# Performance work log

Hardware: AMD Instinct MI355X
Metric: run time of the kernel (lower is better)

The kernel has to match this reference:

```python
import jax, jax.numpy as jnp
import numpy as np

B, L, C = 32, 64, 4


def setup_inputs() -> dict:
    key = jax.random.key(0)
    k_idx, k0, k1, k2, k3 = jax.random.split(key, 5)
    # One-hot encoded sequences, flattened to (B, L*C) as the layer expects.
    idx = jax.random.randint(k_idx, (B, L), 0, C)
    x_lc = jax.nn.one_hot(idx, C, dtype=jnp.float32).reshape(B, L * C)
    return {
        "x_lc": x_lc,
        "theta_0": jnp.zeros((1,), dtype=jnp.float32),  # Constant(0.0) init
        "theta_1": 0.05 * jax.random.normal(k1, (L, C), dtype=jnp.float32),
        "theta_2": 0.05 * jax.random.normal(k2, (L, C, L, C), dtype=jnp.float32),
        "theta_3": 0.05 * jax.random.normal(k3, (L, C, L, C, L, C), dtype=jnp.float32),
    }


def reference(x_lc, theta_0, theta_1, theta_2, theta_3):
    Lp, Cp = theta_1.shape
    xr = x_lc.reshape(-1, Lp, Cp)  # (B, L, C)
    pos = jnp.arange(Lp)
    # strict upper-triangular position masks: l0 < l1 (< l2)
    m2 = (pos[None, :] > pos[:, None]).astype(theta_2.dtype)      # (L, L)
    m3 = m2[:, :, None] * m2[None, :, :]                           # (L, L, L)
    # order 1: sum_{l,c} theta_1[l,c] x[b,l,c]
    phi = theta_0[0] + jnp.einsum('ua,bua->b', theta_1, xr)
    # order 2: sum over l0<l1 of theta_2 * x x
    phi = phi + jnp.einsum('uavc,uv,bua,bvc->b', theta_2, m2, xr, xr)
    # order 3: sum over l0<l1<l2 of theta_3 * x x x
    phi = phi + jnp.einsum('uavcwe,uvw,bua,bvc,bwe->b', theta_3, m3, xr, xr, xr)
    return phi.reshape(-1, 1)
```

## Files before the change

kernel.cpp:

```cpp
#include <hip/hip_runtime.h>

#define BB 32
#define LL 64
#define LC 256
#define NPAIR 2016
#define WSTRIDE 2048

__global__ __launch_bounds__(256) void pair_kernel(
    const float* __restrict__ x, const float* __restrict__ t2,
    const float* __restrict__ t3, float* __restrict__ ws2)
{
    const int t = blockIdx.x;
    int v = (int)((1.0f + sqrtf(8.0f * (float)t + 1.0f)) * 0.5f);
    while (v * (v - 1) / 2 > t) --v;
    while ((v + 1) * v / 2 <= t) ++v;
    const int u = t - v * (v - 1) / 2;

    const int tid = threadIdx.x;
    const int b = tid >> 3, k = tid & 7;
    const float4* __restrict__ x4 = (const float4*)x + b * 64;

    int c[8];
#pragma unroll
    for (int m = 0; m < 8; ++m) {
        float4 f = x4[8 * m + k];
        int ci = 0; float best = f.x;
        if (f.y > best) { best = f.y; ci = 1; }
        if (f.z > best) { best = f.z; ci = 2; }
        if (f.w > best) { best = f.w; ci = 3; }
        c[m] = ci;
    }
    float4 fu = x4[u], fv = x4[v];
    int cu = 0; { float bst = fu.x;
        if (fu.y > bst) { bst = fu.y; cu = 1; }
        if (fu.z > bst) { bst = fu.z; cu = 2; }
        if (fu.w > bst) { bst = fu.w; cu = 3; } }
    int cv = 0; { float bst = fv.x;
        if (fv.y > bst) { bst = fv.y; cv = 1; }
        if (fv.z > bst) { bst = fv.z; cv = 2; }
        if (fv.w > bst) { bst = fv.w; cv = 3; } }
    const int pu = 4 * u + cu, pv = 4 * v + cv;

    const float4* __restrict__ row4 =
        (const float4*)(t3 + ((size_t)pu << 16) + ((size_t)pv << 8));

    float acc = 0.0f;
    const int mstart = (v + 1 - k + 7) >> 3;
#pragma unroll
    for (int m = 0; m < 8; ++m) {
        if (m >= mstart) {
            float4 f = row4[8 * m + k];
            float s0 = (c[m] & 2) ? f.z : f.x;
            float s1 = (c[m] & 2) ? f.w : f.y;
            acc += (c[m] & 1) ? s1 : s0;
        }
    }
    acc += __shfl_down(acc, 4, 8);
    acc += __shfl_down(acc, 2, 8);
    acc += __shfl_down(acc, 1, 8);
    if (k == 0) ws2[b * WSTRIDE + t] = acc + t2[pu * LC + pv];
}

__global__ __launch_bounds__(256) void reduce_kernel(
    const float* __restrict__ x, const float* __restrict__ t0,
    const float* __restrict__ t1, const float* __restrict__ ws2,
    float* __restrict__ out)
{
    const int b = blockIdx.x;
    const int tid = threadIdx.x;
    const float* __restrict__ wsb = ws2 + b * WSTRIDE;
    float v = 0.0f;
    for (int t = tid; t < NPAIR; t += 256) v += wsb[t];
    if (tid < LL) {
        float4 f = ((const float4*)x)[b * 64 + tid];
        int c = 0; float best = f.x;
        if (f.y > best) { best = f.y; c = 1; }
        if (f.z > best) { best = f.z; c = 2; }
        if (f.w > best) { best = f.w; c = 3; }
        v += t1[4 * tid + c];
    }
    for (int off = 32; off > 0; off >>= 1) v += __shfl_down(v, off, 64);
    __shared__ float wsum[4];
    if ((tid & 63) == 0) wsum[tid >> 6] = v;
    __syncthreads();
    if (tid == 0) out[b] = wsum[0] + wsum[1] + wsum[2] + wsum[3] + t0[0];
}

extern "C" void kernel_launch(void* const* d_in, const int* in_sizes, int n_in,
                              void* d_out, int out_size, void* d_ws, size_t ws_size,
                              hipStream_t stream) {
    const float* x  = (const float*)d_in[0];
    const float* t0 = (const float*)d_in[1];
    const float* t1 = (const float*)d_in[2];
    const float* t2 = (const float*)d_in[3];
    const float* t3 = (const float*)d_in[4];
    float* out = (float*)d_out;
    float* ws2 = (float*)d_ws;

    pair_kernel<<<NPAIR, 256, 0, stream>>>(x, t2, t3, ws2);
    reduce_kernel<<<BB, 256, 0, stream>>>(x, t0, t1, ws2, out);
}
```

Measured before the change: 104.7 us.

## Fuse pair and reduce kernels with atomics, process four pairs per block

Merges the two-kernel pipeline into one kernel that walks four consecutive (u,v) pairs per block, reuses the decoded one-hot codes across them, and accumulates straight into the output with atomicAdd after a memset. The aim is to remove the workspace round trip and the second launch, and to cut per-block setup relative to the useful gathers. In exchange there are 504 blocks instead of 2016, which lowers parallelism for the memory-bound gathers, adds a memset launch, and introduces contended atomics on 32 outputs.

Result: slower. 115.5 us (+10.3%).

```diff
diff --git a/kernel.cpp b/kernel.cpp
--- a/kernel.cpp
+++ b/kernel.cpp
@@ -4,18 +4,15 @@
 #define LL 64
 #define LC 256
 #define NPAIR 2016
-#define WSTRIDE 2048
+#define PPB 4
+#define NBLK (NPAIR / PPB)
 
-__global__ __launch_bounds__(256) void pair_kernel(
-    const float* __restrict__ x, const float* __restrict__ t2,
-    const float* __restrict__ t3, float* __restrict__ ws2)
+__global__ __launch_bounds__(256) void fused_kernel(
+    const float* __restrict__ x, const float* __restrict__ t0,
+    const float* __restrict__ t1, const float* __restrict__ t2,
+    const float* __restrict__ t3, float* __restrict__ out)
 {
-    const int t = blockIdx.x;
-    int v = (int)((1.0f + sqrtf(8.0f * (float)t + 1.0f)) * 0.5f);
-    while (v * (v - 1) / 2 > t) --v;
-    while ((v + 1) * v / 2 <= t) ++v;
-    const int u = t - v * (v - 1) / 2;
-
+    const int g = blockIdx.x;
     const int tid = threadIdx.x;
     const int b = tid >> 3, k = tid & 7;
     const float4* __restrict__ x4 = (const float4*)x + b * 64;
@@ -30,60 +27,57 @@
         if (f.w > best) { best = f.w; ci = 3; }
         c[m] = ci;
     }
-    float4 fu = x4[u], fv = x4[v];
-    int cu = 0; { float bst = fu.x;
-        if (fu.y > bst) { bst = fu.y; cu = 1; }
-        if (fu.z > bst) { bst = fu.z; cu = 2; }
-        if (fu.w > bst) { bst = fu.w; cu = 3; } }
-    int cv = 0; { float bst = fv.x;
-        if (fv.y > bst) { bst = fv.y; cv = 1; }
-        if (fv.z > bst) { bst = fv.z; cv = 2; }
-        if (fv.w > bst) { bst = fv.w; cv = 3; } }
-    const int pu = 4 * u + cu, pv = 4 * v + cv;
 
-    const float4* __restrict__ row4 =
-        (const float4*)(t3 + ((size_t)pu << 16) + ((size_t)pv << 8));
+    int t = g * PPB;
+    int v = (int)((1.0f + sqrtf(8.0f * (float)t + 1.0f)) * 0.5f);
+    while (v * (v - 1) / 2 > t) --v;
+    while ((v + 1) * v / 2 <= t) ++v;
+    int u = t - v * (v - 1) / 2;
 
     float acc = 0.0f;
-    const int mstart = (v + 1 - k + 7) >> 3;
 #pragma unroll
-    for (int m = 0; m < 8; ++m) {
-        if (m >= mstart) {
-            float4 f = row4[8 * m + k];
-            float s0 = (c[m] & 2) ? f.z : f.x;
-            float s1 = (c[m] & 2) ? f.w : f.y;
-            acc += (c[m] & 1) ? s1 : s0;
+    for (int p = 0; p < PPB; ++p) {
+        float4 fu = x4[u], fv = x4[v];
+        int cu = 0; { float bst = fu.x;
+            if (fu.y > bst) { bst = fu.y; cu = 1; }
+            if (fu.z > bst) { bst = fu.z; cu = 2; }
+            if (fu.w > bst) { bst = fu.w; cu = 3; } }
+        int cv = 0; { float bst = fv.x;
+            if (fv.y > bst) { bst = fv.y; cv = 1; }
+            if (fv.z > bst) { bst = fv.z; cv = 2; }
+            if (fv.w > bst) { bst = fv.w; cv = 3; } }
+        const int pu = 4 * u + cu, pv = 4 * v + cv;
+
+        const float4* __restrict__ row4 =
+            (const float4*)(t3 + ((size_t)pu << 16) + ((size_t)pv << 8));
+        const int mstart = (v + 1 - k + 7) >> 3;
+#pragma unroll
+        for (int m = 0; m < 8; ++m) {
+            if (m >= mstart) {
+                float4 f = row4[8 * m + k];
+                float s0 = (c[m] & 2) ? f.z : f.x;
+                float s1 = (c[m] & 2) ? f.w : f.y;
+                acc += (c[m] & 1) ? s1 : s0;
+            }
         }
+        if (k == 0) acc += t2[pu * LC + pv];
+
+        ++u; if (u == v) { u = 0; ++v; }
     }
+
+    if (g == 0) {
+#pragma unroll
+        for (int m = 0; m < 8; ++m)
+            acc += t1[4 * (8 * m + k) + c[m]];
+    }
+
     acc += __shfl_down(acc, 4, 8);
     acc += __shfl_down(acc, 2, 8);
     acc += __shfl_down(acc, 1, 8);
-    if (k == 0) ws2[b * WSTRIDE + t] = acc + t2[pu * LC + pv];
-}
-
-__global__ __launch_bounds__(256) void reduce_kernel(
-    const float* __restrict__ x, const float* __restrict__ t0,
-    const float* __restrict__ t1, const float* __restrict__ ws2,
-    float* __restrict__ out)
-{
-    const int b = blockIdx.x;
-    const int tid = threadIdx.x;
-    const float* __restrict__ wsb = ws2 + b * WSTRIDE;
-    float v = 0.0f;
-    for (int t = tid; t < NPAIR; t += 256) v += wsb[t];
-    if (tid < LL) {
-        float4 f = ((const float4*)x)[b * 64 + tid];
-        int c = 0; float best = f.x;
-        if (f.y > best) { best = f.y; c = 1; }
-        if (f.z > best) { best = f.z; c = 2; }
-        if (f.w > best) { best = f.w; c = 3; }
-        v += t1[4 * tid + c];
+    if (k == 0) {
+        if (g == 0) acc += t0[0];
+        atomicAdd(&out[b], acc);
     }
-    for (int off = 32; off > 0; off >>= 1) v += __shfl_down(v, off, 64);
-    __shared__ float wsum[4];
-    if ((tid & 63) == 0) wsum[tid >> 6] = v;
-    __syncthreads();
-    if (tid == 0) out[b] = wsum[0] + wsum[1] + wsum[2] + wsum[3] + t0[0];
 }
 
 extern "C" void kernel_launch(void* const* d_in, const int* in_sizes, int n_in,
@@ -95,8 +89,7 @@
     const float* t2 = (const float*)d_in[3];
     const float* t3 = (const float*)d_in[4];
     float* out = (float*)d_out;
-    float* ws2 = (float*)d_ws;
 
-    pair_kernel<<<NPAIR, 256, 0, stream>>>(x, t2, t3, ws2);
-    reduce_kernel<<<BB, 256, 0, stream>>>(x, t0, t1, ws2, out);
+    hipMemsetAsync(out, 0, BB * sizeof(float), stream);
+    fused_kernel<<<NBLK, 256, 0, stream>>>(x, t0, t1, t2, t3, out);
 }
```
